# Optimization experiments

Hardware: AMD Instinct MI355X
Metric: run time of the kernel (lower is better)

## Reference

```python
import jax, jax.numpy as jnp
import numpy as np

B = 16384      # batch
N = 128        # number of DNPU nodes (experts)
I = 3          # data electrodes per node
C = 4          # control electrodes per node
E = I + C      # total electrodes = 7
H = 90         # surrogate-model hidden width
L = 3          # number of extra hidden layers


def setup_inputs() -> dict:
    key = jax.random.key(0)
    ks = jax.random.split(key, 8)
    s_in = 1.0 / np.sqrt(E)
    s_h = 1.0 / np.sqrt(H)
    return {
        "x": jax.random.normal(ks[0], (B, N * I), dtype=jnp.float32),
        "controls": jax.random.uniform(ks[1], (N, C), dtype=jnp.float32, minval=-1.2, maxval=0.6),
        "W_in": jax.random.normal(ks[2], (N, E, H), dtype=jnp.float32) * s_in,
        "b_in": jax.random.normal(ks[3], (N, H), dtype=jnp.float32) * 0.1,
        "W_hid": jax.random.normal(ks[4], (L, N, H, H), dtype=jnp.float32) * s_h,
        "b_hid": jax.random.normal(ks[5], (L, N, H), dtype=jnp.float32) * 0.1,
        "W_out": jax.random.normal(ks[6], (N, H), dtype=jnp.float32) * s_h,
        "b_out": jax.random.normal(ks[7], (N,), dtype=jnp.float32) * 0.1,
    }


def reference(x, controls, W_in, b_in, W_hid, b_hid, W_out, b_out):
    # DNPU_Layer: partition x into N chunks of I, each node merges its data
    # electrodes with its learned control voltages into a 7-electrode vector,
    # evaluates the shared surrogate MLP with per-node parameters, outputs 1
    # current per node; results are concatenated along dim 1 -> [B, N].
    b = x.shape[0]
    xd = x.reshape(b, N, I)                                   # partition_input
    ctrl = jnp.broadcast_to(controls[None], (b, N, C))        # per-node controls
    e = jnp.concatenate([xd, ctrl], axis=-1)                  # [B, N, E]
    h = jax.nn.relu(jnp.einsum('bne,neh->bnh', e, W_in) + b_in)
    for l in range(L):  # fixed small layer count
        h = jax.nn.relu(jnp.einsum('bnh,nhk->bnk', h, W_hid[l]) + b_hid[l])
    out = jnp.einsum('bnh,nh->bn', h, W_out) + b_out          # [B, N]
    return out
```

## Files before the change

### kernel.cpp

```cpp
#include <hip/hip_runtime.h>
#include <stdint.h>

namespace {
constexpr int kB  = 16384;
constexpr int kN  = 128;
constexpr int kI  = 3;
constexpr int kC  = 4;
constexpr int kH  = 90;
constexpr int kL  = 3;
constexpr int KP  = 96;
constexpr int FB_PER_NODE = 57;
constexpr int NODE_USH    = FB_PER_NODE * 512;
constexpr size_t WT_BYTES = (size_t)kN * NODE_USH * 2;
constexpr size_t WO_OFF   = WT_BYTES;
constexpr size_t XK_OFF   = WO_OFF + (size_t)kN * KP * 4;
}

typedef __attribute__((ext_vector_type(8))) short bf16x8;
typedef __attribute__((ext_vector_type(16))) float f32x16;

__device__ __forceinline__ uint32_t pack_bf16(float lo, float hi) {
#if __has_builtin(__builtin_amdgcn_cvt_pk_bf16_f32)
  auto r = __builtin_amdgcn_cvt_pk_bf16_f32(lo, hi);
  union { decltype(r) v; uint32_t u; } c; c.v = r; return c.u;
#else
  union { float f; uint32_t i; } a, b; a.f = lo; b.f = hi;
  uint32_t ua = a.i + 0x8000u;
  uint32_t ub = b.i + 0x8000u;
  return __builtin_amdgcn_perm(ub, ua, 0x07060302);
#endif
}
__device__ __forceinline__ ushort f2bf(float f) {
  union { float f; uint32_t i; } v; v.f = f;
  uint32_t u = v.i + 0x7FFFu + ((v.i >> 16) & 1u);
  return (ushort)(u >> 16);
}

__device__ __forceinline__ void pl32swap(uint32_t& a, uint32_t& b) {
#if __has_builtin(__builtin_amdgcn_permlane32_swap)
  auto r = __builtin_amdgcn_permlane32_swap(a, b, false, false);
  a = (uint32_t)r[0]; b = (uint32_t)r[1];
#else
  uint32_t sa = (uint32_t)__shfl_xor((int)a, 32);
  uint32_t sb = (uint32_t)__shfl_xor((int)b, 32);
  bool lo = (threadIdx.x & 63) < 32;
  uint32_t na = lo ? a : sb;
  uint32_t nb = lo ? sa : b;
  a = na; b = nb;
#endif
}

__device__ __forceinline__ void stage16(const ushort* g, ushort* l) {
  __builtin_amdgcn_global_load_lds(
      (const __attribute__((address_space(1))) void*)g,
      (__attribute__((address_space(3))) void*)l, 16, 0, 0);
}

__global__ __launch_bounds__(256) void prep_kernel(
    const float* __restrict__ x,
    const float* __restrict__ W_in, const float* __restrict__ b_in,
    const float* __restrict__ W_hid, const float* __restrict__ b_hid,
    const float* __restrict__ W_out, const float* __restrict__ b_out,
    ushort* __restrict__ wt, float* __restrict__ wo, ushort* __restrict__ xk)
{
  __shared__ float smem[kH * (kH + 1) + kH];
  const int tid = threadIdx.x;
  const int bid = blockIdx.x;

  if (bid < 4 * kN) {
    float* ldsw = smem;
    float* ldsb = smem + kH * (kH + 1);
    const int node  = bid & (kN - 1);
    const int layer = bid >> 7;
    const int ksrc  = (layer == 0) ? (kI + kC) : kH;
    const float* src;
    const float* bsrc;
    if (layer == 0) { src = W_in + (size_t)node * (kI + kC) * kH; bsrc = b_in + (size_t)node * kH; }
    else {
      int l = layer - 1;
      src  = W_hid + (size_t)(l * kN + node) * kH * kH;
      bsrc = b_hid + (size_t)(l * kN + node) * kH;
    }
    for (int idx = tid; idx < ksrc * kH; idx += 256)
      ldsw[(idx / kH) * (kH + 1) + (idx % kH)] = src[idx];
    if (tid < kH) ldsb[tid] = bsrc[tid];
    __syncthreads();
    ushort* dstbase = wt + (size_t)node * NODE_USH
                    + (size_t)((layer == 0) ? 0 : 3 + (layer - 1) * 18) * 512;
    const int nch = (layer == 0) ? 192 : 1152;
#pragma unroll
    for (int it = 0; it < 5; ++it) {
      int c = tid + it * 256;
      if (c < nch) {
        int fb = c >> 6, lane = c & 63;
        int ks = (layer == 0) ? 0 : fb / 3;
        int mt = (layer == 0) ? fb : fb % 3;
        int j  = mt * 32 + (lane & 31);
        int kb = ks * 16 + (lane >> 5) * 8;
        float v[8];
#pragma unroll
        for (int i = 0; i < 8; ++i) {
          int k = kb + i;
          float t = 0.f;
          if (j < kH) {
            if (k < ksrc)       t = ldsw[k * (kH + 1) + j];
            else if (k == ksrc) t = ldsb[j];
          }
          v[i] = t;
        }
        uint4 p;
        p.x = pack_bf16(v[0], v[1]); p.y = pack_bf16(v[2], v[3]);
        p.z = pack_bf16(v[4], v[5]); p.w = pack_bf16(v[6], v[7]);
        *(uint4*)&dstbase[(size_t)c * 8] = p;
      }
    }
  } else if (bid < 4 * kN + 4) {
    int base = (bid - 4 * kN) * 3072;
    for (int t = 0; t < 12; ++t) {
      int idx = base + t * 256 + tid;
      int node = idx / KP, j = idx % KP;
      float v = 0.f;
      if (j < kH)       v = W_out[node * kH + j];
      else if (j == kH) v = b_out[node];
      wo[idx] = v;
    }
  } else {
    int xb = bid - (4 * kN + 4);
    int b0 = (xb & 255) * 64;
    int c0 = (xb >> 8) * 96;
    float* lds = smem;
    for (int idx = tid; idx < 64 * 96; idx += 256) {
      int r = idx / 96, c = idx % 96;
      lds[r * 97 + c] = x[(size_t)(b0 + r) * (kN * kI) + c0 + c];
    }
    __syncthreads();
#pragma unroll
    for (int it = 0; it < 3; ++it) {
      int c = tid + it * 256;
      int nk = c >> 3, b = (c & 7) * 8;
      float v[8];
#pragma unroll
      for (int i = 0; i < 8; ++i) v[i] = lds[(b + i) * 97 + nk];
      uint4 p;
      p.x = pack_bf16(v[0], v[1]); p.y = pack_bf16(v[2], v[3]);
      p.z = pack_bf16(v[4], v[5]); p.w = pack_bf16(v[6], v[7]);
      *(uint4*)&xk[(size_t)(c0 + nk) * kB + b0 + b] = p;
    }
  }
}

__global__ __launch_bounds__(256, 4) void dnpu_kernel(
    const ushort* __restrict__ xk, const float* __restrict__ controls,
    const ushort* __restrict__ wt, const float* __restrict__ wo,
    float* __restrict__ out)
{
  __shared__ __align__(16) ushort wbuf[2][18 * 512];

  const int tid  = threadIdx.x;
  const int lane = tid & 63;
  const int wid  = tid >> 6;
  const int node = (int)(blockIdx.x & 127);
  const int m0   = (int)(blockIdx.x >> 7) * 128 + wid * 32;
  const int col  = lane & 31;
  const int hh   = lane >> 5;

  const ushort* wnode = wt + (size_t)node * NODE_USH;

  auto stage_hid = [&](int l, ushort* buf) {
    const ushort* src = wnode + (size_t)(3 + l * 18) * 512;
#pragma unroll
    for (int r = 0; r < 4; ++r)
      stage16(src + (size_t)(r * 256 + wid * 64 + lane) * 8,
              buf + (size_t)(r * 256 + wid * 64) * 8);
    if (wid < 2)
      stage16(src + (size_t)(1024 + wid * 64 + lane) * 8,
              buf + (size_t)(1024 + wid * 64) * 8);
  };

  if (wid < 3)
    stage16(wnode + (size_t)(wid * 64 + lane) * 8, &wbuf[0][(size_t)(wid * 64) * 8]);
  stage_hid(0, &wbuf[1][0]);

  const f32x16 zf = (f32x16)0.0f;

  bf16x8 b0;
  {
    const ushort cb0 = f2bf(controls[node * kC + 0]);
    const ushort cb1 = f2bf(controls[node * kC + 1]);
    const ushort cb2 = f2bf(controls[node * kC + 2]);
    const ushort cb3 = f2bf(controls[node * kC + 3]);
    const ushort* xp = xk + (size_t)node * kI * kB + m0 + col;
    union { ushort s[8]; bf16x8 v; } f;
    f.s[0] = xp[0 * kB];
    f.s[1] = xp[1 * kB];
    f.s[2] = xp[2 * kB];
    f.s[3] = cb0; f.s[4] = cb1; f.s[5] = cb2; f.s[6] = cb3;
    f.s[7] = 0x3F80;
    bf16x8 z = (bf16x8){0,0,0,0,0,0,0,0};
    b0 = hh ? z : f.v;
  }

  union BF { uint32_t u[4]; bf16x8 v; };
  BF Bc[6], Bn[6];

  auto pack_mt = [&](int mt, const f32x16& ae, const f32x16& ao, BF* Bout) {
    float v[16];
#pragma unroll
    for (int r = 0; r < 16; ++r) v[r] = fmaxf(ae[r] + ao[r], 0.f);
    if (mt == 2) v[14] = (hh == 0) ? 1.0f : v[14];
    uint32_t P[8];
#pragma unroll
    for (int w = 0; w < 8; ++w) P[w] = pack_bf16(v[2 * w], v[2 * w + 1]);
    uint32_t q0 = P[0], q2 = P[2]; pl32swap(q0, q2);
    uint32_t q1 = P[1], q3 = P[3]; pl32swap(q1, q3);
    uint32_t q4 = P[4], q6 = P[6]; pl32swap(q4, q6);
    uint32_t q5 = P[5], q7 = P[7]; pl32swap(q5, q7);
    Bout[2 * mt].u[0] = q0; Bout[2 * mt].u[1] = q1;
    Bout[2 * mt].u[2] = q2; Bout[2 * mt].u[3] = q3;
    Bout[2 * mt + 1].u[0] = q4; Bout[2 * mt + 1].u[1] = q5;
    Bout[2 * mt + 1].u[2] = q6; Bout[2 * mt + 1].u[3] = q7;
  };

  auto hidden = [&](const ushort* buf, BF* Bin, BF* Bout) {
#pragma unroll
    for (int mt = 0; mt < 3; ++mt) {
      f32x16 ae, ao;
      __builtin_amdgcn_s_setprio(1);
#pragma unroll
      for (int kp = 0; kp < 3; ++kp) {
        bf16x8 af0 = *(const bf16x8*)&buf[(size_t)((2 * kp) * 3 + mt) * 512 + lane * 8];
        bf16x8 af1 = *(const bf16x8*)&buf[(size_t)((2 * kp + 1) * 3 + mt) * 512 + lane * 8];
        ae = __builtin_amdgcn_mfma_f32_32x32x16_bf16(af0, Bin[2 * kp].v,
                                                     kp ? ae : zf, 0, 0, 0);
        ao = __builtin_amdgcn_mfma_f32_32x32x16_bf16(af1, Bin[2 * kp + 1].v,
                                                     kp ? ao : zf, 0, 0, 0);
      }
      __builtin_amdgcn_s_setprio(0);
      pack_mt(mt, ae, ao, Bout);
    }
  };

  __syncthreads();

  {
#pragma unroll
    for (int mt = 0; mt < 3; ++mt) {
      bf16x8 afr = *(const bf16x8*)&wbuf[0][(size_t)mt * 512 + lane * 8];
      __builtin_amdgcn_s_setprio(1);
      f32x16 a0 = __builtin_amdgcn_mfma_f32_32x32x16_bf16(afr, b0, zf, 0, 0, 0);
      __builtin_amdgcn_s_setprio(0);
      pack_mt(mt, a0, zf, Bc);
    }
  }

  __syncthreads();
  stage_hid(1, &wbuf[0][0]);
  hidden(&wbuf[1][0], Bc, Bn);

  __syncthreads();
  stage_hid(2, &wbuf[1][0]);
  hidden(&wbuf[0][0], Bn, Bc);

  __syncthreads();

  {
    const float* wop = wo + node * KP;
    float s0 = 0.f;
#pragma unroll
    for (int mt = 0; mt < 3; ++mt) {
      f32x16 ae, ao;
      __builtin_amdgcn_s_setprio(1);
#pragma unroll
      for (int kp = 0; kp < 3; ++kp) {
        bf16x8 af0 = *(const bf16x8*)&wbuf[1][(size_t)((2 * kp) * 3 + mt) * 512 + lane * 8];
        bf16x8 af1 = *(const bf16x8*)&wbuf[1][(size_t)((2 * kp + 1) * 3 + mt) * 512 + lane * 8];
        ae = __builtin_amdgcn_mfma_f32_32x32x16_bf16(af0, Bc[2 * kp].v,
                                                     kp ? ae : zf, 0, 0, 0);
        ao = __builtin_amdgcn_mfma_f32_32x32x16_bf16(af1, Bc[2 * kp + 1].v,
                                                     kp ? ao : zf, 0, 0, 0);
      }
      __builtin_amdgcn_s_setprio(0);
#pragma unroll
      for (int g = 0; g < 4; ++g) {
        float4 wf = *(const float4*)&wop[mt * 32 + g * 8 + hh * 4];
#pragma unroll
        for (int r2 = 0; r2 < 4; ++r2) {
          int r = g * 4 + r2;
          float w = (r2 == 0) ? wf.x : (r2 == 1) ? wf.y : (r2 == 2) ? wf.z : wf.w;
          float hv = fmaxf(ae[r] + ao[r], 0.f);
          if (mt == 2 && r == 14)
            hv = (hh == 0) ? 1.0f : hv;
          s0 += hv * w;
        }
      }
    }
    s0 += __shfl_xor(s0, 32);
    if (hh == 0)
      out[(size_t)(m0 + col) * kN + node] = s0;
  }
}

extern "C" void kernel_launch(void* const* d_in, const int* in_sizes, int n_in,
                              void* d_out, int out_size, void* d_ws, size_t ws_size,
                              hipStream_t stream) {
  const float* x        = (const float*)d_in[0];
  const float* controls = (const float*)d_in[1];
  const float* W_in     = (const float*)d_in[2];
  const float* b_in     = (const float*)d_in[3];
  const float* W_hid    = (const float*)d_in[4];
  const float* b_hid    = (const float*)d_in[5];
  const float* W_out    = (const float*)d_in[6];
  const float* b_out    = (const float*)d_in[7];
  float* out = (float*)d_out;

  ushort* wt = (ushort*)d_ws;
  float*  wo = (float*)((char*)d_ws + WO_OFF);
  ushort* xk = (ushort*)((char*)d_ws + XK_OFF);

  hipLaunchKernelGGL(prep_kernel, dim3(4 * kN + 4 + 1024), dim3(256), 0, stream,
                     x, W_in, b_in, W_hid, b_hid, W_out, b_out, wt, wo, xk);

  dim3 grid((kB / 128) * kN);
  hipLaunchKernelGGL(dnpu_kernel, grid, dim3(256), 0, stream,
                     xk, controls, wt, wo, out);
}
```

Measured before the change: 224.4 us.

## Single-buffer LDS weights, single accumulator chain, raise occupancy to five blocks

Drops the LDS double buffer in favour of one 18KB weight buffer, staged synchronously with extra barriers before each hidden layer. Each MFMA tile now accumulates along one six-step chain instead of two interleaved even/odd chains, which frees accumulator registers. Launch bounds rise from 4 to 5 blocks per CU. The aim is higher occupancy from lower LDS and register use. The cost is serialized weight loads with no prefetch overlap and longer dependent MFMA chains.

```diff
diff --git a/kernel.cpp b/kernel.cpp
--- a/kernel.cpp
+++ b/kernel.cpp
@@ -149,12 +149,12 @@
   }
 }
 
-__global__ __launch_bounds__(256, 4) void dnpu_kernel(
+__global__ __launch_bounds__(256, 5) void dnpu_kernel(
     const ushort* __restrict__ xk, const float* __restrict__ controls,
     const ushort* __restrict__ wt, const float* __restrict__ wo,
     float* __restrict__ out)
 {
-  __shared__ __align__(16) ushort wbuf[2][18 * 512];
+  __shared__ __align__(16) ushort wbuf[18 * 512];
 
   const int tid  = threadIdx.x;
   const int lane = tid & 63;
@@ -166,20 +166,19 @@
 
   const ushort* wnode = wt + (size_t)node * NODE_USH;
 
-  auto stage_hid = [&](int l, ushort* buf) {
+  auto stage_hid = [&](int l) {
     const ushort* src = wnode + (size_t)(3 + l * 18) * 512;
 #pragma unroll
     for (int r = 0; r < 4; ++r)
       stage16(src + (size_t)(r * 256 + wid * 64 + lane) * 8,
-              buf + (size_t)(r * 256 + wid * 64) * 8);
+              wbuf + (size_t)(r * 256 + wid * 64) * 8);
     if (wid < 2)
       stage16(src + (size_t)(1024 + wid * 64 + lane) * 8,
-              buf + (size_t)(1024 + wid * 64) * 8);
+              wbuf + (size_t)(1024 + wid * 64) * 8);
   };
 
   if (wid < 3)
-    stage16(wnode + (size_t)(wid * 64 + lane) * 8, &wbuf[0][(size_t)(wid * 64) * 8]);
-  stage_hid(0, &wbuf[1][0]);
+    stage16(wnode + (size_t)(wid * 64 + lane) * 8, &wbuf[(size_t)(wid * 64) * 8]);
 
   const f32x16 zf = (f32x16)0.0f;
 
@@ -203,10 +202,10 @@
   union BF { uint32_t u[4]; bf16x8 v; };
   BF Bc[6], Bn[6];
 
-  auto pack_mt = [&](int mt, const f32x16& ae, const f32x16& ao, BF* Bout) {
+  auto pack_mt = [&](int mt, const f32x16& a, BF* Bout) {
     float v[16];
 #pragma unroll
-    for (int r = 0; r < 16; ++r) v[r] = fmaxf(ae[r] + ao[r], 0.f);
+    for (int r = 0; r < 16; ++r) v[r] = fmaxf(a[r], 0.f);
     if (mt == 2) v[14] = (hh == 0) ? 1.0f : v[14];
     uint32_t P[8];
 #pragma unroll
@@ -221,22 +220,19 @@
     Bout[2 * mt + 1].u[2] = q6; Bout[2 * mt + 1].u[3] = q7;
   };
 
-  auto hidden = [&](const ushort* buf, BF* Bin, BF* Bout) {
+  auto hidden = [&](BF* Bin, BF* Bout) {
 #pragma unroll
     for (int mt = 0; mt < 3; ++mt) {
-      f32x16 ae, ao;
+      f32x16 a;
       __builtin_amdgcn_s_setprio(1);
 #pragma unroll
-      for (int kp = 0; kp < 3; ++kp) {
-        bf16x8 af0 = *(const bf16x8*)&buf[(size_t)((2 * kp) * 3 + mt) * 512 + lane * 8];
-        bf16x8 af1 = *(const bf16x8*)&buf[(size_t)((2 * kp + 1) * 3 + mt) * 512 + lane * 8];
-        ae = __builtin_amdgcn_mfma_f32_32x32x16_bf16(af0, Bin[2 * kp].v,
-                                                     kp ? ae : zf, 0, 0, 0);
-        ao = __builtin_amdgcn_mfma_f32_32x32x16_bf16(af1, Bin[2 * kp + 1].v,
-                                                     kp ? ao : zf, 0, 0, 0);
+      for (int ks = 0; ks < 6; ++ks) {
+        bf16x8 afr = *(const bf16x8*)&wbuf[(size_t)(ks * 3 + mt) * 512 + lane * 8];
+        a = __builtin_amdgcn_mfma_f32_32x32x16_bf16(afr, Bin[ks].v,
+                                                    ks ? a : zf, 0, 0, 0);
       }
       __builtin_amdgcn_s_setprio(0);
-      pack_mt(mt, ae, ao, Bout);
+      pack_mt(mt, a, Bout);
     }
   };
 
@@ -245,22 +241,24 @@
   {
 #pragma unroll
     for (int mt = 0; mt < 3; ++mt) {
-      bf16x8 afr = *(const bf16x8*)&wbuf[0][(size_t)mt * 512 + lane * 8];
-      __builtin_amdgcn_s_setprio(1);
-      f32x16 a0 = __builtin_amdgcn_mfma_f32_32x32x16_bf16(afr, b0, zf, 0, 0, 0);
-      __builtin_amdgcn_s_setprio(0);
-      pack_mt(mt, a0, zf, Bc);
+      bf16x8 afr = *(const bf16x8*)&wbuf[(size_t)mt * 512 + lane * 8];
+      f32x16 a = __builtin_amdgcn_mfma_f32_32x32x16_bf16(afr, b0, zf, 0, 0, 0);
+      pack_mt(mt, a, Bc);
     }
   }
 
   __syncthreads();
-  stage_hid(1, &wbuf[0][0]);
-  hidden(&wbuf[1][0], Bc, Bn);
-
-  __syncthreads();
-  stage_hid(2, &wbuf[1][0]);
-  hidden(&wbuf[0][0], Bn, Bc);
-
+  stage_hid(0);
+  __syncthreads();
+  hidden(Bc, Bn);
+
+  __syncthreads();
+  stage_hid(1);
+  __syncthreads();
+  hidden(Bn, Bc);
+
+  __syncthreads();
+  stage_hid(2);
   __syncthreads();
 
   {
@@ -268,16 +266,13 @@
     float s0 = 0.f;
 #pragma unroll
     for (int mt = 0; mt < 3; ++mt) {
-      f32x16 ae, ao;
+      f32x16 a;
       __builtin_amdgcn_s_setprio(1);
 #pragma unroll
-      for (int kp = 0; kp < 3; ++kp) {
-        bf16x8 af0 = *(const bf16x8*)&wbuf[1][(size_t)((2 * kp) * 3 + mt) * 512 + lane * 8];
-        bf16x8 af1 = *(const bf16x8*)&wbuf[1][(size_t)((2 * kp + 1) * 3 + mt) * 512 + lane * 8];
-        ae = __builtin_amdgcn_mfma_f32_32x32x16_bf16(af0, Bc[2 * kp].v,
-                                                     kp ? ae : zf, 0, 0, 0);
-        ao = __builtin_amdgcn_mfma_f32_32x32x16_bf16(af1, Bc[2 * kp + 1].v,
-                                                     kp ? ao : zf, 0, 0, 0);
+      for (int ks = 0; ks < 6; ++ks) {
+        bf16x8 afr = *(const bf16x8*)&wbuf[(size_t)(ks * 3 + mt) * 512 + lane * 8];
+        a = __builtin_amdgcn_mfma_f32_32x32x16_bf16(afr, Bc[ks].v,
+                                                    ks ? a : zf, 0, 0, 0);
       }
       __builtin_amdgcn_s_setprio(0);
 #pragma unroll
@@ -287,7 +282,7 @@
         for (int r2 = 0; r2 < 4; ++r2) {
           int r = g * 4 + r2;
           float w = (r2 == 0) ? wf.x : (r2 == 1) ? wf.y : (r2 == 2) ? wf.z : wf.w;
-          float hv = fmaxf(ae[r] + ao[r], 0.f);
+          float hv = fmaxf(a[r], 0.f);
           if (mt == 2 && r == 14)
             hv = (hh == 0) ? 1.0f : hv;
           s0 += hv * w;
```

Measured after the change: 222.7 us. Within noise of the previous version (-0.8%).
